# Kernel optimization log

Measured on AMD Instinct MI355X. Metric: run time of the kernel, lower is better.

The kernel has to match this reference:

```python
import jax, jax.numpy as jnp
from jax import lax
import numpy as np

V = 50000   # location_size
H = 512     # hidden_size (embedding width == LSTM width in original code)
B = 128     # number of ragged sequences (batch)
L = 512     # max sequence length (padded)


def setup_inputs() -> dict:
    key = jax.random.key(0)
    ks = jax.random.split(key, 8)
    tokens = jax.random.randint(ks[0], (B, L), 0, V)           # assembled ragged token ids, padded
    lengths = jax.random.randint(ks[1], (B,), 1, L + 1)        # valid length per sequence (>=1)
    s = 1.0 / np.sqrt(H)
    emb = jax.random.normal(ks[2], (V, H), jnp.float32)
    W_ih = jax.random.uniform(ks[3], (4 * H, H), jnp.float32, -s, s)
    W_hh = jax.random.uniform(ks[4], (4 * H, H), jnp.float32, -s, s)
    b_ih = jax.random.uniform(ks[5], (4 * H,), jnp.float32, -s, s)
    b_hh = jax.random.uniform(ks[6], (4 * H,), jnp.float32, -s, s)
    W_fc = jax.random.uniform(ks[7], (V, H), jnp.float32, -s, s)
    b_fc = jnp.zeros((V,), jnp.float32)
    return {"tokens": tokens, "lengths": lengths, "emb": emb,
            "W_ih": W_ih, "W_hh": W_hh, "b_ih": b_ih, "b_hh": b_hh,
            "W_fc": W_fc, "b_fc": b_fc}


def reference(tokens, lengths, emb, W_ih, W_hh, b_ih, b_hh, W_fc, b_fc):
    # Embedding gather (the ragged per-trajectory slice+concat collapses to this gather)
    x = emb[tokens]                                             # [B, L, H]
    # Precompute input contribution to gates once: [B, L, 4H]
    x_proj = jnp.einsum('blh,gh->blg', x, W_ih) + b_ih + b_hh
    h0 = jnp.zeros((B, H), x.dtype)
    c0 = jnp.zeros((B, H), x.dtype)

    def step(carry, inp):
        h, c = carry
        xp, t = inp                                             # xp: [B, 4H]
        gates = xp + h @ W_hh.T
        i, f, g, o = jnp.split(gates, 4, axis=-1)               # PyTorch gate order i,f,g,o
        i = jax.nn.sigmoid(i)
        f = jax.nn.sigmoid(f)
        g = jnp.tanh(g)
        o = jax.nn.sigmoid(o)
        c_new = f * c + i * g
        h_new = o * jnp.tanh(c_new)
        valid = (t < lengths)[:, None]                          # freeze state past each length
        return (jnp.where(valid, h_new, h), jnp.where(valid, c_new, c)), None

    (hT, _), _ = lax.scan(step, (h0, c0),
                          (jnp.swapaxes(x_proj, 0, 1), jnp.arange(L)))
    # fc on final hidden state of (single) last layer, squeeze(0) of [1,B,H] -> [B,H]
    return hT @ W_fc.T + b_fc                                    # [B, V]
```

## Files before the change

### kernel.cpp

```cpp
#include <hip/hip_runtime.h>
#include <stdint.h>


#define NB   128
#define LMAX 512
#define HD   512
#define G4   2048
#define NV   50000

#define H0C_OFF     0
#define T0_OFF      131072
#define T1_OFF      393216
#define C_OFF       655360
#define EMB16_OFF   917504
#define EMB16_BYTES (NV * HD * 2)
#define WIH16_OFF   (EMB16_OFF + EMB16_BYTES)
#define WIH16_BYTES (G4 * HD * 2)
#define XP_OFF      (WIH16_OFF + WIH16_BYTES)
#define INIT_W4     57344

typedef _Float16 f16;
typedef _Float16 half8  __attribute__((ext_vector_type(8)));
typedef float    float4v __attribute__((ext_vector_type(4)));
typedef uint32_t u32;
typedef unsigned long long u64;
typedef uint32_t u32x4 __attribute__((ext_vector_type(4)));

__device__ __forceinline__ half8 cvt8(const float* p) {
  float4v a = *(const float4v*)p;
  float4v b = *(const float4v*)(p + 4);
  half8 r;
  r[0] = (f16)a[0]; r[1] = (f16)a[1]; r[2] = (f16)a[2]; r[3] = (f16)a[3];
  r[4] = (f16)b[0]; r[5] = (f16)b[1]; r[6] = (f16)b[2]; r[7] = (f16)b[3];
  return r;
}
__device__ __forceinline__ float sigmoidf_(float x) { return 1.0f / (1.0f + __expf(-x)); }
__device__ __forceinline__ float tanhf_(float x)    { return 1.0f - 2.0f / (1.0f + __expf(2.0f * x)); }

__device__ __forceinline__ void barx() {
  __builtin_amdgcn_sched_barrier(0);
  __builtin_amdgcn_s_waitcnt(0xC07F);
  __builtin_amdgcn_s_barrier();
  __builtin_amdgcn_sched_barrier(0);
}

extern "C" __global__ void k0_init(u32x4* ws4) {
  int idx = blockIdx.x * 256 + threadIdx.x;
  u32x4 z = {0u, 0u, 0u, 0u};
  if (idx < INIT_W4) ws4[idx] = z;
}

extern "C" __global__ void __launch_bounds__(256)
k_cvt(const float* __restrict__ src, f16* __restrict__ dst, int n8) {
  int i = blockIdx.x * 256 + threadIdx.x;
  if (i >= n8) return;
  ((half8*)dst)[i] = cvt8(src + (size_t)i * 8);
}

extern "C" __global__ void __launch_bounds__(256)
k1_xproj(const int* __restrict__ tokens, const int* __restrict__ lengths,
         const f16* __restrict__ emb16, const f16* __restrict__ wih16,
         const float* __restrict__ bih, const float* __restrict__ bhh,
         f16* __restrict__ xp, int t0c, int TC) {
  int b  = blockIdx.x;
  int mt = blockIdx.y;
  int nt = blockIdx.z;
  int len = lengths[b];
  int t0 = t0c + mt * 64;
  if (t0 >= len) return;

  __shared__ f16 As[64 * 512];
  int tid = threadIdx.x;

  #pragma unroll
  for (int it = 0; it < 16; ++it) {
    int gl = tid + 256 * it;
    int row = gl >> 6, gi = gl & 63;
    int tok = tokens[b * LMAX + t0 + row];
    half8 v = *(const half8*)(emb16 + (size_t)tok * HD + gi * 8);
    *(half8*)&As[row * 512 + ((gi ^ (row & 7)) * 8)] = v;
  }
  __syncthreads();

  int wave = tid >> 6, lane = tid & 63;
  int quad = lane >> 4, l15 = lane & 15;
  int col0 = nt * 128 + wave * 32;

  float4v acc[4][2] = {};
  for (int c = 0; c < 16; ++c) {
    half8 b0 = *(const half8*)(wih16 + (size_t)(col0 + l15) * HD + c * 32 + quad * 8);
    half8 b1 = *(const half8*)(wih16 + (size_t)(col0 + 16 + l15) * HD + c * 32 + quad * 8);
    #pragma unroll
    for (int mm = 0; mm < 4; ++mm) {
      int row = mm * 16 + l15;
      half8 a = *(const half8*)&As[row * 512 + (((c * 4 + quad) ^ (row & 7)) * 8)];
      acc[mm][0] = __builtin_amdgcn_mfma_f32_16x16x32_f16(a, b0, acc[mm][0], 0, 0, 0);
      acc[mm][1] = __builtin_amdgcn_mfma_f32_16x16x32_f16(a, b1, acc[mm][1], 0, 0, 0);
    }
  }

  #pragma unroll
  for (int q = 0; q < 2; ++q) {
    int gcol = col0 + q * 16 + l15;
    float bias = bih[gcol] + bhh[gcol];
    #pragma unroll
    for (int mm = 0; mm < 4; ++mm) {
      #pragma unroll
      for (int j = 0; j < 4; ++j) {
        int t = t0 + mm * 16 + quad * 4 + j;
        if (t < len)
          xp[((size_t)b * TC + (t - t0c)) * G4 + gcol] = (f16)(acc[mm][q][j] + bias);
      }
    }
  }
}

extern "C" __global__ void __launch_bounds__(256, 1)
k2_lstm(const int* __restrict__ lengths, const float* __restrict__ Whh,
        const f16* __restrict__ xp, u64* __restrict__ tb0, u64* __restrict__ tb1,
        f16* __restrict__ h0c, float* __restrict__ cbuf, int t0c, int TC) {
  int wg = blockIdx.x;
  int grp = wg & 7, memb = wg >> 3;
  int s0 = grp * 16;
  int tid = threadIdx.x;

  int gm = 0;
  for (int i = 0; i < 16; ++i) { int l = lengths[s0 + i]; gm = l > gm ? l : gm; }
  int tend = (t0c + TC < gm) ? (t0c + TC) : gm;
  if (t0c >= tend) return;

  __shared__ f16 Hs[16 * 512];
  __shared__ float gS[16][133];

  int wave = tid >> 6, lane = tid & 63;
  int quad = lane >> 4, l15 = lane & 15;

  half8 wf0[16], wf1[16];
  {
    const float* r0 = Whh + (size_t)(wave * 512 + memb * 32 + l15) * HD;
    const float* r1 = r0 + (size_t)16 * HD;
    #pragma unroll
    for (int c = 0; c < 16; ++c) {
      wf0[c] = cvt8(r0 + c * 32 + quad * 8);
      wf1[c] = cvt8(r1 + c * 32 + quad * 8);
    }
  }

  int sE = tid >> 4, kE = tid & 15, kk0 = kE * 2;
  int len = lengths[s0 + sE];
  float c0 = cbuf[(size_t)(s0 + sE) * HD + memb * 32 + kk0];
  float c1 = cbuf[(size_t)(s0 + sE) * HD + memb * 32 + kk0 + 1];

  size_t wIdx = (size_t)(s0 + sE) * 256 + memb * 16 + kE;
  const u64* hin0 = (t0c & 1) ? tb1 : tb0;
  u32 hp = (u32)hin0[wIdx];

  int gG = tid >> 2, w4 = (tid & 3) * 2;

  u64 a[16];
  #pragma unroll
  for (int r = 0; r < 16; ++r)
    a[r] = __hip_atomic_load(hin0 + (size_t)(s0 + r) * 256 + tid,
                             __ATOMIC_RELAXED, __HIP_MEMORY_SCOPE_AGENT);

  for (int t = t0c; t < tend; ++t) {
    const u64* tin  = (t & 1) ? tb1 : tb0;
    u64*       tout = (t & 1) ? tb0 : tb1;
    u32 tg = (u32)t;

    u32 x4[4];
    {
      const f16* p = xp + ((size_t)(s0 + sE) * TC + (t - t0c)) * G4 + memb * 32 + kk0;
      x4[0] = *(const u32*)p;          x4[1] = *(const u32*)(p + 512);
      x4[2] = *(const u32*)(p + 1024); x4[3] = *(const u32*)(p + 1536);
    }

    for (;;) {
      u32 bad = 0;
      #pragma unroll
      for (int r = 0; r < 16; ++r)
        bad |= ((u32)(a[r] >> 32) != tg) ? (1u << r) : 0u;
      if (!bad) break;
      __builtin_amdgcn_s_sleep(1);
      #pragma unroll
      for (int r = 0; r < 16; ++r)
        if (bad & (1u << r))
          a[r] = __hip_atomic_load(tin + (size_t)(s0 + r) * 256 + tid,
                                   __ATOMIC_RELAXED, __HIP_MEMORY_SCOPE_AGENT);
    }

    #pragma unroll
    for (int r = 0; r < 16; ++r)
      *(u32*)&Hs[r * 512 + ((gG ^ (r & 7)) << 3) + w4] = (u32)a[r];
    barx();

    float4v a0e = {}, a0o = {}, a1e = {}, a1o = {};
    #pragma unroll
    for (int c = 0; c < 16; ++c) {
      half8 av = *(const half8*)&Hs[l15 * 512 + (((c * 4 + quad) ^ (l15 & 7)) * 8)];
      if (c & 1) {
        a0o = __builtin_amdgcn_mfma_f32_16x16x32_f16(av, wf0[c], a0o, 0, 0, 0);
        a1o = __builtin_amdgcn_mfma_f32_16x16x32_f16(av, wf1[c], a1o, 0, 0, 0);
      } else {
        a0e = __builtin_amdgcn_mfma_f32_16x16x32_f16(av, wf0[c], a0e, 0, 0, 0);
        a1e = __builtin_amdgcn_mfma_f32_16x16x32_f16(av, wf1[c], a1e, 0, 0, 0);
      }
    }
    float4v g0 = a0e + a0o, g1 = a1e + a1o;
    #pragma unroll
    for (int j = 0; j < 4; ++j) {
      gS[quad * 4 + j][wave * 32 + l15]      = g0[j];
      gS[quad * 4 + j][wave * 32 + 16 + l15] = g1[j];
    }
    barx();

    if (t < len) {
      union { u32 u; f16 h[2]; } xi, xf, xg, xo, hpk;
      xi.u = x4[0]; xf.u = x4[1]; xg.u = x4[2]; xo.u = x4[3];
      float i0 = sigmoidf_(gS[sE][kk0]          + (float)xi.h[0]);
      float i1 = sigmoidf_(gS[sE][kk0 + 1]      + (float)xi.h[1]);
      float f0 = sigmoidf_(gS[sE][32 + kk0]     + (float)xf.h[0]);
      float f1 = sigmoidf_(gS[sE][32 + kk0 + 1] + (float)xf.h[1]);
      float q0 = tanhf_  (gS[sE][64 + kk0]      + (float)xg.h[0]);
      float q1 = tanhf_  (gS[sE][64 + kk0 + 1]  + (float)xg.h[1]);
      float o0 = sigmoidf_(gS[sE][96 + kk0]     + (float)xo.h[0]);
      float o1 = sigmoidf_(gS[sE][96 + kk0 + 1] + (float)xo.h[1]);
      c0 = f0 * c0 + i0 * q0;
      c1 = f1 * c1 + i1 * q1;
      hpk.h[0] = (f16)(o0 * tanhf_(c0));
      hpk.h[1] = (f16)(o1 * tanhf_(c1));
      hp = hpk.u;
    }
    u64 wv = ((u64)(u32)(t + 1) << 32) | (u64)hp;
    __hip_atomic_store(tout + wIdx, wv, __ATOMIC_RELAXED, __HIP_MEMORY_SCOPE_AGENT);

    if (t + 1 < tend) {
      #pragma unroll
      for (int r = 0; r < 16; ++r)
        a[r] = __hip_atomic_load(tout + (size_t)(s0 + r) * 256 + tid,
                                 __ATOMIC_RELAXED, __HIP_MEMORY_SCOPE_AGENT);
    }
  }

  cbuf[(size_t)(s0 + sE) * HD + memb * 32 + kk0]     = c0;
  cbuf[(size_t)(s0 + sE) * HD + memb * 32 + kk0 + 1] = c1;

  *(u32*)&h0c[(size_t)(s0 + sE) * HD + memb * 32 + kk0] = hp;
}

extern "C" __global__ void __launch_bounds__(256)
k3_fc(const f16* __restrict__ hT, const float* __restrict__ Wfc,
      const float* __restrict__ bfc, float* __restrict__ out) {
  int tid = threadIdx.x;
  int wave = tid >> 6, lane = tid & 63, quad = lane >> 4, l15 = lane & 15;
  int v = blockIdx.x * 64 + wave * 16 + l15;
  int vc = v < NV ? v : NV - 1;
  float4v acc[8] = {};
  for (int c = 0; c < 16; ++c) {
    half8 bfr = cvt8(Wfc + (size_t)vc * HD + c * 32 + quad * 8);
    #pragma unroll
    for (int mt = 0; mt < 8; ++mt) {
      half8 afr = *(const half8*)&hT[(size_t)(mt * 16 + l15) * HD + c * 32 + quad * 8];
      acc[mt] = __builtin_amdgcn_mfma_f32_16x16x32_f16(afr, bfr, acc[mt], 0, 0, 0);
    }
  }
  if (v < NV) {
    float bias = bfc[v];
    #pragma unroll
    for (int mt = 0; mt < 8; ++mt)
      #pragma unroll
      for (int j = 0; j < 4; ++j)
        out[(size_t)(mt * 16 + quad * 4 + j) * NV + v] = acc[mt][j] + bias;
  }
}

extern "C" void kernel_launch(void* const* d_in, const int* in_sizes, int n_in,
                              void* d_out, int out_size, void* d_ws, size_t ws_size,
                              hipStream_t stream) {
  (void)in_sizes; (void)n_in; (void)out_size;
  const int*   tokens  = (const int*)d_in[0];
  const int*   lengths = (const int*)d_in[1];
  const float* emb     = (const float*)d_in[2];
  const float* Wih     = (const float*)d_in[3];
  const float* Whh     = (const float*)d_in[4];
  const float* bih     = (const float*)d_in[5];
  const float* bhh     = (const float*)d_in[6];
  const float* Wfc     = (const float*)d_in[7];
  const float* bfc     = (const float*)d_in[8];
  float* out = (float*)d_out;
  char* ws = (char*)d_ws;

  f16*  h0c  = (f16*)(ws + H0C_OFF);
  u64*  tb0  = (u64*)(ws + T0_OFF);
  u64*  tb1  = (u64*)(ws + T1_OFF);
  float* cbuf = (float*)(ws + C_OFF);
  f16* emb16 = (f16*)(ws + EMB16_OFF);
  f16* wih16 = (f16*)(ws + WIH16_OFF);
  f16* xp    = (f16*)(ws + XP_OFF);

  int TC = 512;
  while (TC > 64 && (size_t)XP_OFF + (size_t)NB * TC * G4 * 2 > ws_size) TC >>= 1;

  hipLaunchKernelGGL(k0_init, dim3(224), dim3(256), 0, stream, (u32x4*)ws);
  hipLaunchKernelGGL(k_cvt, dim3((NV * HD / 8 + 255) / 256), dim3(256), 0, stream,
                     emb, emb16, NV * HD / 8);
  hipLaunchKernelGGL(k_cvt, dim3((G4 * HD / 8 + 255) / 256), dim3(256), 0, stream,
                     Wih, wih16, G4 * HD / 8);
  for (int t0 = 0; t0 < LMAX; t0 += TC) {
    hipLaunchKernelGGL(k1_xproj, dim3(NB, TC / 64, 16), dim3(256), 0, stream,
                       tokens, lengths, emb16, wih16, bih, bhh, xp, t0, TC);
    hipLaunchKernelGGL(k2_lstm, dim3(128), dim3(256), 0, stream,
                       lengths, Whh, xp, tb0, tb1, h0c, cbuf, t0, TC);
  }
  hipLaunchKernelGGL(k3_fc, dim3((NV + 63) / 64), dim3(256), 0, stream,
                     h0c, Wfc, bfc, out);
}
```

Measured before the change: 2.164 ms.

## Use XCC-local cache-scoped polling when all group members share one XCC

Each LSTM workgroup records its XCC id from a hardware register, and each 16-member group checks whether all members landed on the same XCC. If so, the cross-workgroup hidden-state exchange uses sc0-scoped loads and stores, which stay in the shared L2 instead of going through agent-scope coherent paths, lowering per-step sync latency. A fallback re-publishes the current and previous state with agent-scope stores after 64 failed spins. Polling now reloads all 16 rows and waits on vmcnt each iteration. This relies on undocumented XCC-id register semantics and on the assumption that sc0 accesses are coherent within one XCC.

```diff
diff --git a/kernel.cpp b/kernel.cpp
--- a/kernel.cpp
+++ b/kernel.cpp
@@ -12,12 +12,13 @@
 #define T0_OFF      131072
 #define T1_OFF      393216
 #define C_OFF       655360
-#define EMB16_OFF   917504
+#define XCC_OFF     917504
+#define EMB16_OFF   921600
 #define EMB16_BYTES (NV * HD * 2)
 #define WIH16_OFF   (EMB16_OFF + EMB16_BYTES)
 #define WIH16_BYTES (G4 * HD * 2)
 #define XP_OFF      (WIH16_OFF + WIH16_BYTES)
-#define INIT_W4     57344
+#define INIT_W4     57600
 
 typedef _Float16 f16;
 typedef _Float16 half8  __attribute__((ext_vector_type(8)));
@@ -42,6 +43,19 @@
   __builtin_amdgcn_s_waitcnt(0xC07F);
   __builtin_amdgcn_s_barrier();
   __builtin_amdgcn_sched_barrier(0);
+}
+
+__device__ __forceinline__ void ld16f(u64* a, const u64* base) {
+  #pragma unroll
+  for (int r = 0; r < 16; ++r)
+    asm volatile("global_load_dwordx2 %0, %1, off sc0"
+                 : "=v"(a[r]) : "v"(base + (size_t)r * 256) : "memory");
+}
+__device__ __forceinline__ void ld16s(u64* a, const u64* base) {
+  #pragma unroll
+  for (int r = 0; r < 16; ++r)
+    a[r] = __hip_atomic_load(base + (size_t)r * 256,
+                             __ATOMIC_RELAXED, __HIP_MEMORY_SCOPE_AGENT);
 }
 
 extern "C" __global__ void k0_init(u32x4* ws4) {
@@ -118,7 +132,8 @@
 extern "C" __global__ void __launch_bounds__(256, 1)
 k2_lstm(const int* __restrict__ lengths, const float* __restrict__ Whh,
         const f16* __restrict__ xp, u64* __restrict__ tb0, u64* __restrict__ tb1,
-        f16* __restrict__ h0c, float* __restrict__ cbuf, int t0c, int TC) {
+        f16* __restrict__ h0c, float* __restrict__ cbuf, u32* __restrict__ xcc,
+        int ci, int t0c, int TC) {
   int wg = blockIdx.x;
   int grp = wg & 7, memb = wg >> 3;
   int s0 = grp * 16;
@@ -129,8 +144,15 @@
   int tend = (t0c + TC < gm) ? (t0c + TC) : gm;
   if (t0c >= tend) return;
 
+  u32* slot = xcc + ci * NB;
+  if (tid == 0) {
+    u32 id = __builtin_amdgcn_s_getreg((3u << 11) | 20u) & 0xFu;
+    __hip_atomic_store(slot + wg, id + 1u, __ATOMIC_RELAXED, __HIP_MEMORY_SCOPE_AGENT);
+  }
+
   __shared__ f16 Hs[16 * 512];
   __shared__ float gS[16][133];
+  __shared__ u32 fastS;
 
   int wave = tid >> 6, lane = tid & 63;
   int quad = lane >> 4, l15 = lane & 15;
@@ -146,6 +168,22 @@
     }
   }
 
+  if (tid == 0) {
+    u32 mn = 255u, mx = 0u;
+    for (;;) {
+      mn = 255u; mx = 0u;
+      #pragma unroll
+      for (int m = 0; m < 16; ++m) {
+        u32 v = __hip_atomic_load(slot + grp + 8 * m,
+                                  __ATOMIC_RELAXED, __HIP_MEMORY_SCOPE_AGENT);
+        mn = v < mn ? v : mn; mx = v > mx ? v : mx;
+      }
+      if (mn != 0u) break;
+      __builtin_amdgcn_s_sleep(8);
+    }
+    fastS = (mn == mx) ? 1u : 0u;
+  }
+
   int sE = tid >> 4, kE = tid & 15, kk0 = kE * 2;
   int len = lengths[s0 + sE];
   float c0 = cbuf[(size_t)(s0 + sE) * HD + memb * 32 + kk0];
@@ -155,17 +193,21 @@
   const u64* hin0 = (t0c & 1) ? tb1 : tb0;
   u32 hp = (u32)hin0[wIdx];
 
+  u64 wv_cur  = ((u64)(u32)t0c << 32) | (u64)hp;
+  u64 wv_prev = wv_cur;
+
   int gG = tid >> 2, w4 = (tid & 3) * 2;
 
+  __syncthreads();
+  bool fastR = fastS != 0u;
+
   u64 a[16];
-  #pragma unroll
-  for (int r = 0; r < 16; ++r)
-    a[r] = __hip_atomic_load(hin0 + (size_t)(s0 + r) * 256 + tid,
-                             __ATOMIC_RELAXED, __HIP_MEMORY_SCOPE_AGENT);
+  ld16s(a, hin0 + (size_t)s0 * 256 + tid);
 
   for (int t = t0c; t < tend; ++t) {
     const u64* tin  = (t & 1) ? tb1 : tb0;
     u64*       tout = (t & 1) ? tb0 : tb1;
+    const u64* tinb = tin + (size_t)s0 * 256 + tid;
     u32 tg = (u32)t;
 
     u32 x4[4];
@@ -175,18 +217,26 @@
       x4[2] = *(const u32*)(p + 1024); x4[3] = *(const u32*)(p + 1536);
     }
 
-    for (;;) {
-      u32 bad = 0;
-      #pragma unroll
-      for (int r = 0; r < 16; ++r)
-        bad |= ((u32)(a[r] >> 32) != tg) ? (1u << r) : 0u;
-      if (!bad) break;
-      __builtin_amdgcn_s_sleep(1);
-      #pragma unroll
-      for (int r = 0; r < 16; ++r)
-        if (bad & (1u << r))
-          a[r] = __hip_atomic_load(tin + (size_t)(s0 + r) * 256 + tid,
-                                   __ATOMIC_RELAXED, __HIP_MEMORY_SCOPE_AGENT);
+    {
+      int spin = 0;
+      for (;;) {
+        asm volatile("s_waitcnt vmcnt(0)" ::: "memory");
+        __builtin_amdgcn_sched_barrier(0);
+        u32 bad = 0;
+        #pragma unroll
+        for (int r = 0; r < 16; ++r)
+          bad |= ((u32)(a[r] >> 32) != tg) ? 1u : 0u;
+        if (!bad) break;
+        if (fastR && t != t0c && ++spin == 64) {
+          fastR = false;
+          __hip_atomic_store((u64*)tin + wIdx, wv_cur,
+                             __ATOMIC_RELAXED, __HIP_MEMORY_SCOPE_AGENT);
+          __hip_atomic_store(tout + wIdx, wv_prev,
+                             __ATOMIC_RELAXED, __HIP_MEMORY_SCOPE_AGENT);
+        }
+        __builtin_amdgcn_s_sleep(1);
+        if (fastR) ld16f(a, tinb); else ld16s(a, tinb);
+      }
     }
 
     #pragma unroll
@@ -232,13 +282,16 @@
       hp = hpk.u;
     }
     u64 wv = ((u64)(u32)(t + 1) << 32) | (u64)hp;
-    __hip_atomic_store(tout + wIdx, wv, __ATOMIC_RELAXED, __HIP_MEMORY_SCOPE_AGENT);
+    wv_prev = wv_cur; wv_cur = wv;
+    if (fastR)
+      asm volatile("global_store_dwordx2 %0, %1, off sc0"
+                   :: "v"(tout + wIdx), "v"(wv) : "memory");
+    else
+      __hip_atomic_store(tout + wIdx, wv, __ATOMIC_RELAXED, __HIP_MEMORY_SCOPE_AGENT);
 
     if (t + 1 < tend) {
-      #pragma unroll
-      for (int r = 0; r < 16; ++r)
-        a[r] = __hip_atomic_load(tout + (size_t)(s0 + r) * 256 + tid,
-                                 __ATOMIC_RELAXED, __HIP_MEMORY_SCOPE_AGENT);
+      const u64* toutb = tout + (size_t)s0 * 256 + tid;
+      if (fastR) ld16f(a, toutb); else ld16s(a, toutb);
     }
   }
 
@@ -294,6 +347,7 @@
   u64*  tb0  = (u64*)(ws + T0_OFF);
   u64*  tb1  = (u64*)(ws + T1_OFF);
   float* cbuf = (float*)(ws + C_OFF);
+  u32*  xcc  = (u32*)(ws + XCC_OFF);
   f16* emb16 = (f16*)(ws + EMB16_OFF);
   f16* wih16 = (f16*)(ws + WIH16_OFF);
   f16* xp    = (f16*)(ws + XP_OFF);
@@ -301,7 +355,7 @@
   int TC = 512;
   while (TC > 64 && (size_t)XP_OFF + (size_t)NB * TC * G4 * 2 > ws_size) TC >>= 1;
 
-  hipLaunchKernelGGL(k0_init, dim3(224), dim3(256), 0, stream, (u32x4*)ws);
+  hipLaunchKernelGGL(k0_init, dim3(225), dim3(256), 0, stream, (u32x4*)ws);
   hipLaunchKernelGGL(k_cvt, dim3((NV * HD / 8 + 255) / 256), dim3(256), 0, stream,
                      emb, emb16, NV * HD / 8);
   hipLaunchKernelGGL(k_cvt, dim3((G4 * HD / 8 + 255) / 256), dim3(256), 0, stream,
@@ -310,7 +364,7 @@
     hipLaunchKernelGGL(k1_xproj, dim3(NB, TC / 64, 16), dim3(256), 0, stream,
                        tokens, lengths, emb16, wih16, bih, bhh, xp, t0, TC);
     hipLaunchKernelGGL(k2_lstm, dim3(128), dim3(256), 0, stream,
-                       lengths, Whh, xp, tb0, tb1, h0c, cbuf, t0, TC);
+                       lengths, Whh, xp, tb0, tb1, h0c, cbuf, xcc, t0 / TC, t0, TC);
   }
   hipLaunchKernelGGL(k3_fc, dim3((NV + 63) / 64), dim3(256), 0, stream,
                      h0c, Wfc, bfc, out);
```

Result: slower. 2.999 ms (+38.6%).

## Loop all column tiles per xproj block and apply gate activations in MFMA epilogue

Applied to the files above, without the earlier changes.

The input-projection kernel now loops over all 16 column tiles inside one block, so each block gathers its 64 embedding rows into shared memory once instead of 16 separate blocks each redoing the gather. This trades grid parallelism (16x fewer blocks) for less redundant gather traffic. The LSTM step now adds the precomputed input projection and applies sigmoid or tanh right after the MFMA, before writing to shared memory. This spreads the transcendental work across all lanes and shortens the serial cell-update section on the recurrent critical path.

```diff
diff --git a/kernel.cpp b/kernel.cpp
--- a/kernel.cpp
+++ b/kernel.cpp
@@ -64,7 +64,6 @@
          f16* __restrict__ xp, int t0c, int TC) {
   int b  = blockIdx.x;
   int mt = blockIdx.y;
-  int nt = blockIdx.z;
   int len = lengths[b];
   int t0 = t0c + mt * 64;
   if (t0 >= len) return;
@@ -84,32 +83,35 @@
 
   int wave = tid >> 6, lane = tid & 63;
   int quad = lane >> 4, l15 = lane & 15;
-  int col0 = nt * 128 + wave * 32;
-
-  float4v acc[4][2] = {};
-  for (int c = 0; c < 16; ++c) {
-    half8 b0 = *(const half8*)(wih16 + (size_t)(col0 + l15) * HD + c * 32 + quad * 8);
-    half8 b1 = *(const half8*)(wih16 + (size_t)(col0 + 16 + l15) * HD + c * 32 + quad * 8);
-    #pragma unroll
-    for (int mm = 0; mm < 4; ++mm) {
-      int row = mm * 16 + l15;
-      half8 a = *(const half8*)&As[row * 512 + (((c * 4 + quad) ^ (row & 7)) * 8)];
-      acc[mm][0] = __builtin_amdgcn_mfma_f32_16x16x32_f16(a, b0, acc[mm][0], 0, 0, 0);
-      acc[mm][1] = __builtin_amdgcn_mfma_f32_16x16x32_f16(a, b1, acc[mm][1], 0, 0, 0);
-    }
-  }
-
-  #pragma unroll
-  for (int q = 0; q < 2; ++q) {
-    int gcol = col0 + q * 16 + l15;
-    float bias = bih[gcol] + bhh[gcol];
-    #pragma unroll
-    for (int mm = 0; mm < 4; ++mm) {
-      #pragma unroll
-      for (int j = 0; j < 4; ++j) {
-        int t = t0 + mm * 16 + quad * 4 + j;
-        if (t < len)
-          xp[((size_t)b * TC + (t - t0c)) * G4 + gcol] = (f16)(acc[mm][q][j] + bias);
+
+  for (int nt = 0; nt < 16; ++nt) {
+    int col0 = nt * 128 + wave * 32;
+
+    float4v acc[4][2] = {};
+    for (int c = 0; c < 16; ++c) {
+      half8 b0 = *(const half8*)(wih16 + (size_t)(col0 + l15) * HD + c * 32 + quad * 8);
+      half8 b1 = *(const half8*)(wih16 + (size_t)(col0 + 16 + l15) * HD + c * 32 + quad * 8);
+      #pragma unroll
+      for (int mm = 0; mm < 4; ++mm) {
+        int row = mm * 16 + l15;
+        half8 a = *(const half8*)&As[row * 512 + (((c * 4 + quad) ^ (row & 7)) * 8)];
+        acc[mm][0] = __builtin_amdgcn_mfma_f32_16x16x32_f16(a, b0, acc[mm][0], 0, 0, 0);
+        acc[mm][1] = __builtin_amdgcn_mfma_f32_16x16x32_f16(a, b1, acc[mm][1], 0, 0, 0);
+      }
+    }
+
+    #pragma unroll
+    for (int q = 0; q < 2; ++q) {
+      int gcol = col0 + q * 16 + l15;
+      float bias = bih[gcol] + bhh[gcol];
+      #pragma unroll
+      for (int mm = 0; mm < 4; ++mm) {
+        #pragma unroll
+        for (int j = 0; j < 4; ++j) {
+          int t = t0 + mm * 16 + quad * 4 + j;
+          if (t < len)
+            xp[((size_t)b * TC + (t - t0c)) * G4 + gcol] = (f16)(acc[mm][q][j] + bias);
+        }
       }
     }
   }
@@ -168,11 +170,15 @@
     u64*       tout = (t & 1) ? tb0 : tb1;
     u32 tg = (u32)t;
 
-    u32 x4[4];
+    f16 pxa[4], pxb[4];
     {
-      const f16* p = xp + ((size_t)(s0 + sE) * TC + (t - t0c)) * G4 + memb * 32 + kk0;
-      x4[0] = *(const u32*)p;          x4[1] = *(const u32*)(p + 512);
-      x4[2] = *(const u32*)(p + 1024); x4[3] = *(const u32*)(p + 1536);
+      const f16* xb = xp + (size_t)(t - t0c) * G4 + wave * 512 + memb * 32 + l15;
+      #pragma unroll
+      for (int j = 0; j < 4; ++j) {
+        size_t off = (size_t)(s0 + quad * 4 + j) * TC * G4;
+        pxa[j] = xb[off];
+        pxb[j] = xb[off + 16];
+      }
     }
 
     for (;;) {
@@ -207,26 +213,26 @@
       }
     }
     float4v g0 = a0e + a0o, g1 = a1e + a1o;
+
     #pragma unroll
     for (int j = 0; j < 4; ++j) {
-      gS[quad * 4 + j][wave * 32 + l15]      = g0[j];
-      gS[quad * 4 + j][wave * 32 + 16 + l15] = g1[j];
+      float v0 = g0[j] + (float)pxa[j];
+      float v1 = g1[j] + (float)pxb[j];
+      float u0 = (wave == 2) ? tanhf_(v0) : sigmoidf_(v0);
+      float u1 = (wave == 2) ? tanhf_(v1) : sigmoidf_(v1);
+      gS[quad * 4 + j][wave * 32 + l15]      = u0;
+      gS[quad * 4 + j][wave * 32 + 16 + l15] = u1;
     }
     barx();
 
     if (t < len) {
-      union { u32 u; f16 h[2]; } xi, xf, xg, xo, hpk;
-      xi.u = x4[0]; xf.u = x4[1]; xg.u = x4[2]; xo.u = x4[3];
-      float i0 = sigmoidf_(gS[sE][kk0]          + (float)xi.h[0]);
-      float i1 = sigmoidf_(gS[sE][kk0 + 1]      + (float)xi.h[1]);
-      float f0 = sigmoidf_(gS[sE][32 + kk0]     + (float)xf.h[0]);
-      float f1 = sigmoidf_(gS[sE][32 + kk0 + 1] + (float)xf.h[1]);
-      float q0 = tanhf_  (gS[sE][64 + kk0]      + (float)xg.h[0]);
-      float q1 = tanhf_  (gS[sE][64 + kk0 + 1]  + (float)xg.h[1]);
-      float o0 = sigmoidf_(gS[sE][96 + kk0]     + (float)xo.h[0]);
-      float o1 = sigmoidf_(gS[sE][96 + kk0 + 1] + (float)xo.h[1]);
+      float i0 = gS[sE][kk0],      i1 = gS[sE][kk0 + 1];
+      float f0 = gS[sE][32 + kk0], f1 = gS[sE][32 + kk0 + 1];
+      float q0 = gS[sE][64 + kk0], q1 = gS[sE][64 + kk0 + 1];
+      float o0 = gS[sE][96 + kk0], o1 = gS[sE][96 + kk0 + 1];
       c0 = f0 * c0 + i0 * q0;
       c1 = f1 * c1 + i1 * q1;
+      union { u32 u; f16 h[2]; } hpk;
       hpk.h[0] = (f16)(o0 * tanhf_(c0));
       hpk.h[1] = (f16)(o1 * tanhf_(c1));
       hp = hpk.u;
@@ -307,7 +313,7 @@
   hipLaunchKernelGGL(k_cvt, dim3((G4 * HD / 8 + 255) / 256), dim3(256), 0, stream,
                      Wih, wih16, G4 * HD / 8);
   for (int t0 = 0; t0 < LMAX; t0 += TC) {
-    hipLaunchKernelGGL(k1_xproj, dim3(NB, TC / 64, 16), dim3(256), 0, stream,
+    hipLaunchKernelGGL(k1_xproj, dim3(NB, TC / 64), dim3(256), 0, stream,
                        tokens, lengths, emb16, wih16, bih, bhh, xp, t0, TC);
     hipLaunchKernelGGL(k2_lstm, dim3(128), dim3(256), 0, stream,
                        lengths, Whh, xp, tb0, tb1, h0c, cbuf, t0, TC);
```

Measured after the change: 2.536 ms. 17.2% more time.
